# Kernel optimization log

Hardware: AMD Instinct MI355X
Metric: run time of the kernel (lower is better)

The kernel has to match this reference:

```python
import jax, jax.numpy as jnp
import numpy as np

N, E = 50000, 800000
IN_DIM, HID, OUT_DIM = 128, 64, 64
H1, H2 = 4, 2
LRELU_SLOPE = 0.2
LN_EPS = 1e-5


def _glorot(key, shape):
    fan = shape[0] + shape[-1]
    lim = float(np.sqrt(6.0 / fan))
    return jax.random.uniform(key, shape, jnp.float32, -lim, lim)


def setup_inputs() -> dict:
    key = jax.random.key(0)
    ks = jax.random.split(key, 12)
    x = jax.random.normal(ks[0], (N, IN_DIM), jnp.float32)
    edge_index = jax.random.randint(ks[1], (2, E), 0, N, jnp.int64)
    return {
        "x": x,
        "edge_index": edge_index,
        # layer 1: GATConv(128 -> 64, heads=4, concat=True)
        "W1": _glorot(ks[2], (IN_DIM, H1 * HID)),
        "att_src1": _glorot(ks[3], (H1, HID)),
        "att_dst1": _glorot(ks[4], (H1, HID)),
        "b1": jnp.zeros((H1 * HID,), jnp.float32),
        # LayerNorm(256)
        "ln_w": jnp.ones((H1 * HID,), jnp.float32),
        "ln_b": jnp.zeros((H1 * HID,), jnp.float32),
        # layer 2: GATConv(256 -> 64, heads=2, concat=False)
        "W2": _glorot(ks[5], (H1 * HID, H2 * OUT_DIM)),
        "att_src2": _glorot(ks[6], (H2, OUT_DIM)),
        "att_dst2": _glorot(ks[7], (H2, OUT_DIM)),
        "b2": jnp.zeros((OUT_DIM,), jnp.float32),
    }


def gat_layer(x, src, dst, W, a_src, a_dst, bias, heads, out_ch, concat):
    n = x.shape[0]
    h = (x @ W).reshape(n, heads, out_ch)                 # [N,H,C]
    al_s = jnp.einsum("nhc,hc->nh", h, a_src)             # [N,H]
    al_d = jnp.einsum("nhc,hc->nh", h, a_dst)
    e = jax.nn.leaky_relu(al_s[src] + al_d[dst], LRELU_SLOPE)  # [E,H]
    # segment softmax over incoming edges of each dst node
    m = jax.ops.segment_max(e, dst, num_segments=n)
    e = jnp.exp(e - m[dst])
    denom = jax.ops.segment_sum(e, dst, num_segments=n)
    alpha = e / denom[dst]                                # [E,H]
    msg = h[src] * alpha[:, :, None]                      # [E,H,C]
    out = jax.ops.segment_sum(msg, dst, num_segments=n)   # [N,H,C]
    out = out.reshape(n, heads * out_ch) if concat else out.mean(axis=1)
    return out + bias


def layer_norm(x, w, b):
    mu = x.mean(axis=-1, keepdims=True)
    var = ((x - mu) ** 2).mean(axis=-1, keepdims=True)
    return (x - mu) * jax.lax.rsqrt(var + LN_EPS) * w + b


def reference(x, edge_index, W1, att_src1, att_dst1, b1, ln_w, ln_b,
              W2, att_src2, att_dst2, b2):
    # PyG GATConv adds self-loops by default
    loops = jnp.arange(N, dtype=edge_index.dtype)
    src = jnp.concatenate([edge_index[0], loops])
    dst = jnp.concatenate([edge_index[1], loops])
    h = gat_layer(x, src, dst, W1, att_src1, att_dst1, b1, H1, HID, True)
    h = layer_norm(h, ln_w, ln_b)
    h = jax.nn.elu(h)
    # dropout is identity in eval mode
    h = gat_layer(h, src, dst, W2, att_src2, att_dst2, b2, H2, OUT_DIM, False)
    return h
```

## Files before the change

### kernel.cpp

```cpp
#include <hip/hip_runtime.h>
#include <hip/hip_bf16.h>
#include <math.h>

#define IN_DIM  128
#define HID     64
#define H1      4
#define H2      2
#define OUT_DIM 64
#define D1      256
#define D2      128
#define LRELU   0.2f
#define LN_EPS  1e-5f

using short8 = __attribute__((ext_vector_type(8))) short;
using f32x4  = __attribute__((ext_vector_type(4))) float;

static __device__ __forceinline__ unsigned short f2bf_bits(float f)
{
    __hip_bfloat16 b = __float2bfloat16(f);
    return *reinterpret_cast<unsigned short*>(&b);
}
static __device__ __forceinline__ float2 unpack_bf2(unsigned int p)
{
    float2 r;
    r.x = __uint_as_float(p << 16);
    r.y = __uint_as_float(p & 0xffff0000u);
    return r;
}
static __device__ __forceinline__ unsigned int pack_bf2(float x, float y)
{
    return (unsigned int)f2bf_bits(x) | ((unsigned int)f2bf_bits(y) << 16);
}

static __device__ __forceinline__ float lrelu_exp(float v)
{
    v = v > 0.f ? v : LRELU * v;
    return __expf(v);
}

static __device__ __forceinline__ int detect_i64(const int* __restrict__ ei)
{
    int any_odd_nonzero = 0;
    #pragma unroll
    for (int k = 1; k < 16; k += 2) any_odd_nonzero |= (ei[k] != 0);
    return any_odd_nonzero ? 0 : 1;
}

__global__ __launch_bounds__(256) void conv_hist_kernel(
    const float* __restrict__ W1, const float* __restrict__ W2,
    unsigned short* __restrict__ Wp1, unsigned short* __restrict__ Wp2,
    const int* __restrict__ ei, int E, int* __restrict__ deg)
{
    const int bid = blockIdx.x;
    if (bid < 256) {
        int tid = bid * 256 + threadIdx.x;
        if (tid < 32768) {
            int j = tid & 7, l = (tid >> 3) & 63, rest = tid >> 9;
            int s = rest & 15, t = rest >> 4;
            int k = t * 32 + (l >> 4) * 8 + j, col = s * 16 + (l & 15);
            Wp1[tid] = f2bf_bits(W1[k * D1 + col]);
        } else {
            int id = tid - 32768;
            int j = id & 7, l = (id >> 3) & 63, rest = id >> 9;
            int s = rest & 7, t = rest >> 3;
            int k = t * 32 + (l >> 4) * 8 + j, col = s * 16 + (l & 15);
            Wp2[id] = f2bf_bits(W2[k * D2 + col]);
        }
    } else {
        const int i64f = detect_i64(ei);
        int e = (bid - 256) * 256 + threadIdx.x;
        if (e >= E) return;
        int dst = i64f ? ei[2 * ((size_t)E + e)] : ei[E + e];
        atomicAdd(&deg[dst], 1);
    }
}

__global__ __launch_bounds__(256) void scan_gemm1_kernel(
    const int* __restrict__ deg, int N, int* __restrict__ bsum, int scanB,
    const float* __restrict__ x, const unsigned short* __restrict__ Wp,
    const float* __restrict__ att_s, const float* __restrict__ att_d,
    unsigned short* __restrict__ h1b,
    float* __restrict__ al_s, float* __restrict__ al_d)
{
    __shared__ __align__(16) unsigned short As[16 * 136];
    const int tid = threadIdx.x;

    if ((int)blockIdx.x < scanB) {
        int* s = (int*)As;
        int i = blockIdx.x * 256 + tid;
        s[tid] = (i < N) ? deg[i] : 0;
        __syncthreads();
        for (int st = 128; st > 0; st >>= 1) {
            if (tid < st) s[tid] += s[tid + st];
            __syncthreads();
        }
        if (tid == 0) bsum[blockIdx.x] = s[0];
        return;
    }

    const int n0 = ((int)blockIdx.x - scanB) * 16;
    const int l = tid & 63, w = tid >> 6;

    #pragma unroll
    for (int it = 0; it < 2; ++it) {
        int ch = tid + it * 256;
        int r = ch >> 5, c4 = (ch & 31) * 4;
        int row = n0 + r;
        float4 v = (row < N) ? ((const float4*)x)[(size_t)row * 32 + (c4 >> 2)]
                             : make_float4(0.f, 0.f, 0.f, 0.f);
        ushort4 pk = make_ushort4(f2bf_bits(v.x), f2bf_bits(v.y),
                                  f2bf_bits(v.z), f2bf_bits(v.w));
        *(ushort4*)&As[r * 136 + c4] = pk;
    }

    short8 bfr[4][4];
    #pragma unroll
    for (int t = 0; t < 4; ++t)
        #pragma unroll
        for (int p = 0; p < 4; ++p)
            bfr[t][p] = ((const short8*)Wp)[(t * 16 + (w * 4 + p)) * 64 + l];

    __syncthreads();

    f32x4 acc[4] = {{0.f,0.f,0.f,0.f},{0.f,0.f,0.f,0.f},
                    {0.f,0.f,0.f,0.f},{0.f,0.f,0.f,0.f}};
    #pragma unroll
    for (int t = 0; t < 4; ++t) {
        short8 a = *(const short8*)&As[(l & 15) * 136 + t * 32 + (l >> 4) * 8];
        #pragma unroll
        for (int p = 0; p < 4; ++p)
            acc[p] = __builtin_amdgcn_mfma_f32_16x16x32_bf16(a, bfr[t][p], acc[p], 0, 0, 0);
    }

    const int colbase = w * 64 + (l & 15);
    const int rowbase = n0 + (l >> 4) * 4;
    #pragma unroll
    for (int p = 0; p < 4; ++p) {
        int col = colbase + p * 16;
        #pragma unroll
        for (int r = 0; r < 4; ++r) {
            int row = rowbase + r;
            if (row < N) h1b[(size_t)row * D1 + col] = f2bf_bits(acc[p][r]);
        }
    }

    float as_p[4], ad_p[4];
    #pragma unroll
    for (int p = 0; p < 4; ++p) {
        as_p[p] = att_s[colbase + p * 16];
        ad_p[p] = att_d[colbase + p * 16];
    }
    #pragma unroll
    for (int r = 0; r < 4; ++r) {
        float ps = acc[0][r] * as_p[0] + acc[1][r] * as_p[1]
                 + acc[2][r] * as_p[2] + acc[3][r] * as_p[3];
        float pd = acc[0][r] * ad_p[0] + acc[1][r] * ad_p[1]
                 + acc[2][r] * ad_p[2] + acc[3][r] * ad_p[3];
        #pragma unroll
        for (int off = 8; off > 0; off >>= 1) {
            ps += __shfl_down(ps, off);
            pd += __shfl_down(pd, off);
        }
        int row = rowbase + r;
        if ((l & 15) == 0 && row < N) {
            al_s[(size_t)row * H1 + w] = ps;
            al_d[(size_t)row * H1 + w] = pd;
        }
    }
}

__global__ __launch_bounds__(256) void scan_final(
    const int* __restrict__ deg, const int* __restrict__ bsum, int B, int N, int E,
    int* __restrict__ rowptr, int* __restrict__ cursor)
{
    __shared__ int sb[256];
    __shared__ int s[256];
    sb[threadIdx.x] = (threadIdx.x < B) ? bsum[threadIdx.x] : 0;
    __syncthreads();
    for (int st = 1; st < 256; st <<= 1) {
        int t = (threadIdx.x >= st) ? sb[threadIdx.x - st] : 0;
        __syncthreads();
        sb[threadIdx.x] += t;
        __syncthreads();
    }
    const int blockOff = (blockIdx.x == 0) ? 0 : sb[blockIdx.x - 1];

    int i = blockIdx.x * 256 + threadIdx.x;
    int v = (i < N) ? deg[i] : 0;
    s[threadIdx.x] = v;
    __syncthreads();
    for (int st = 1; st < 256; st <<= 1) {
        int t = (threadIdx.x >= st) ? s[threadIdx.x - st] : 0;
        __syncthreads();
        s[threadIdx.x] += t;
        __syncthreads();
    }
    int excl = s[threadIdx.x] - v + blockOff;
    if (i < N) { rowptr[i] = excl; cursor[i] = excl; }
    if (blockIdx.x == 0 && threadIdx.x == 0) rowptr[N] = E;
}

__global__ __launch_bounds__(256) void fill_kernel(
    const int* __restrict__ ei, int E,
    int* __restrict__ cursor, int* __restrict__ csr_src)
{
    const int i64f = detect_i64(ei);
    int e = blockIdx.x * 256 + threadIdx.x;
    if (e >= E) return;
    int src, dst;
    if (i64f) { src = ei[2 * (size_t)e]; dst = ei[2 * ((size_t)E + e)]; }
    else      { src = ei[e];             dst = ei[E + e]; }
    int pos = atomicAdd(&cursor[dst], 1);
    csr_src[pos] = src;
}

__global__ __launch_bounds__(256) void gemm2_mfma(
    const unsigned short* __restrict__ hmidb, const unsigned short* __restrict__ Wp,
    const float* __restrict__ att_s, const float* __restrict__ att_d,
    unsigned short* __restrict__ h2b,
    float* __restrict__ al_s, float* __restrict__ al_d, int N)
{
    __shared__ __align__(16) unsigned short As[16 * 264];
    __shared__ float psL[4][16], pdL[4][16];
    const int tid = threadIdx.x;
    const int n0 = blockIdx.x * 16;
    const int l = tid & 63, w = tid >> 6;

    const short8 zero8 = {0,0,0,0,0,0,0,0};
    #pragma unroll
    for (int it = 0; it < 2; ++it) {
        int ch = tid + it * 256;
        int r = ch >> 5, c8 = (ch & 31) * 8;
        int row = n0 + r;
        short8 v = (row < N) ? ((const short8*)hmidb)[(size_t)row * 32 + (ch & 31)] : zero8;
        *(short8*)&As[r * 264 + c8] = v;
    }

    short8 bfr[8][2];
    #pragma unroll
    for (int t = 0; t < 8; ++t)
        #pragma unroll
        for (int q = 0; q < 2; ++q)
            bfr[t][q] = ((const short8*)Wp)[(t * 8 + (w * 2 + q)) * 64 + l];

    __syncthreads();

    f32x4 acc[2] = {{0.f,0.f,0.f,0.f},{0.f,0.f,0.f,0.f}};
    #pragma unroll
    for (int t = 0; t < 8; ++t) {
        short8 a = *(const short8*)&As[(l & 15) * 264 + t * 32 + (l >> 4) * 8];
        #pragma unroll
        for (int q = 0; q < 2; ++q)
            acc[q] = __builtin_amdgcn_mfma_f32_16x16x32_bf16(a, bfr[t][q], acc[q], 0, 0, 0);
    }

    const int colbase = w * 32 + (l & 15);
    const int rowbase = n0 + (l >> 4) * 4;
    #pragma unroll
    for (int q = 0; q < 2; ++q) {
        int col = colbase + q * 16;
        #pragma unroll
        for (int r = 0; r < 4; ++r) {
            int row = rowbase + r;
            if (row < N) h2b[(size_t)row * D2 + col] = f2bf_bits(acc[q][r]);
        }
    }

    float as_q[2], ad_q[2];
    #pragma unroll
    for (int q = 0; q < 2; ++q) {
        as_q[q] = att_s[colbase + q * 16];
        ad_q[q] = att_d[colbase + q * 16];
    }
    #pragma unroll
    for (int r = 0; r < 4; ++r) {
        float ps = acc[0][r] * as_q[0] + acc[1][r] * as_q[1];
        float pd = acc[0][r] * ad_q[0] + acc[1][r] * ad_q[1];
        #pragma unroll
        for (int off = 8; off > 0; off >>= 1) {
            ps += __shfl_down(ps, off);
            pd += __shfl_down(pd, off);
        }
        if ((l & 15) == 0) {
            psL[w][(l >> 4) * 4 + r] = ps;
            pdL[w][(l >> 4) * 4 + r] = pd;
        }
    }
    __syncthreads();
    if (tid < 32) {
        int rl = tid & 15, hh = tid >> 4;
        int row = n0 + rl;
        if (row < N) {
            al_s[(size_t)row * H2 + hh] = psL[2*hh][rl] + psL[2*hh+1][rl];
            al_d[(size_t)row * H2 + hh] = pdL[2*hh][rl] + pdL[2*hh+1][rl];
        }
    }
}

__global__ __launch_bounds__(64) void agg1_kernel(
    const int* __restrict__ rowptr, const int* __restrict__ csr_src,
    const uint2* __restrict__ h1p,
    const float* __restrict__ al_s, const float* __restrict__ al_d,
    const float* __restrict__ b1,
    const float* __restrict__ ln_w, const float* __restrict__ ln_b,
    uint2* __restrict__ hmidp, int N)
{
    const int n = blockIdx.x;
    const int l = threadIdx.x;
    const int h = l >> 4;
    const float ad = al_d[(size_t)n * H1 + h];

    float a0[4] = {0.f,0.f,0.f,0.f}, a1[4] = {0.f,0.f,0.f,0.f};
    float a2[4] = {0.f,0.f,0.f,0.f}, a3[4] = {0.f,0.f,0.f,0.f};
    float dn0, dn1 = 0.f, dn2 = 0.f, dn3 = 0.f;

    {
        float w = lrelu_exp(al_s[(size_t)n * H1 + h] + ad);
        uint2 p = h1p[(size_t)n * 64 + l];
        float2 va = unpack_bf2(p.x), vb = unpack_bf2(p.y);
        a0[0] = w * va.x; a0[1] = w * va.y; a0[2] = w * vb.x; a0[3] = w * vb.y;
        dn0 = w;
    }

    const int beg = rowptr[n], end = rowptr[n + 1];
    int i = beg;

#define LOADI(k)  int s##k = csr_src[i + k];
#define LOADR(k)  uint2 p##k = h1p[(size_t)s##k * 64 + l]; \
                  float g##k = al_s[(size_t)s##k * H1 + h];
#define WACC(A, D, k) { float w = lrelu_exp(g##k + ad); \
                        float2 va = unpack_bf2(p##k.x), vb = unpack_bf2(p##k.y); \
                        A[0] += w * va.x; A[1] += w * va.y; \
                        A[2] += w * vb.x; A[3] += w * vb.y; D += w; }

    for (; i + 4 <= end; i += 4) {
        LOADI(0) LOADI(1) LOADI(2) LOADI(3)
        LOADR(0) LOADR(1) LOADR(2) LOADR(3)
        WACC(a0, dn0, 0) WACC(a1, dn1, 1) WACC(a2, dn2, 2) WACC(a3, dn3, 3)
    }
    for (; i < end; ++i) {
        LOADI(0) LOADR(0) WACC(a0, dn0, 0)
    }
#undef LOADI
#undef LOADR
#undef WACC

    const float inv = 1.f / ((dn0 + dn1) + (dn2 + dn3));
    float4 bb = ((const float4*)b1)[l];
    float v[4];
    v[0] = ((a0[0]+a1[0]) + (a2[0]+a3[0])) * inv + bb.x;
    v[1] = ((a0[1]+a1[1]) + (a2[1]+a3[1])) * inv + bb.y;
    v[2] = ((a0[2]+a1[2]) + (a2[2]+a3[2])) * inv + bb.z;
    v[3] = ((a0[3]+a1[3]) + (a2[3]+a3[3])) * inv + bb.w;

    float s  = (v[0]+v[1]) + (v[2]+v[3]);
    float s2 = (v[0]*v[0]+v[1]*v[1]) + (v[2]*v[2]+v[3]*v[3]);
    #pragma unroll
    for (int off = 32; off > 0; off >>= 1) {
        s  += __shfl_down(s,  off);
        s2 += __shfl_down(s2, off);
    }
    const float mu   = __shfl(s,  0) * (1.f / 256.f);
    const float ex2  = __shfl(s2, 0) * (1.f / 256.f);
    const float rstd = rsqrtf(ex2 - mu * mu + LN_EPS);
    float4 lw = ((const float4*)ln_w)[l];
    float4 lb = ((const float4*)ln_b)[l];
    float y0 = (v[0] - mu) * rstd * lw.x + lb.x;
    float y1 = (v[1] - mu) * rstd * lw.y + lb.y;
    float y2 = (v[2] - mu) * rstd * lw.z + lb.z;
    float y3 = (v[3] - mu) * rstd * lw.w + lb.w;
    y0 = y0 > 0.f ? y0 : (__expf(y0) - 1.f);
    y1 = y1 > 0.f ? y1 : (__expf(y1) - 1.f);
    y2 = y2 > 0.f ? y2 : (__expf(y2) - 1.f);
    y3 = y3 > 0.f ? y3 : (__expf(y3) - 1.f);
    uint2 outp;
    outp.x = pack_bf2(y0, y1);
    outp.y = pack_bf2(y2, y3);
    hmidp[(size_t)n * 64 + l] = outp;
}

__global__ __launch_bounds__(64) void agg2_kernel(
    const int* __restrict__ rowptr, const int* __restrict__ csr_src,
    const unsigned int* __restrict__ h2p,
    const float* __restrict__ al_s, const float* __restrict__ al_d,
    const float* __restrict__ b2,
    float* __restrict__ out, int N)
{
    const int n = blockIdx.x;
    const int l = threadIdx.x;
    const int h = l >> 5;
    const float ad = al_d[(size_t)n * H2 + h];

    float ax0, ay0, dn0;
    float ax1 = 0.f, ay1 = 0.f, dn1 = 0.f;
    float ax2 = 0.f, ay2 = 0.f, dn2 = 0.f;
    float ax3 = 0.f, ay3 = 0.f, dn3 = 0.f;
    {
        float w = lrelu_exp(al_s[(size_t)n * H2 + h] + ad);
        float2 hv = unpack_bf2(h2p[(size_t)n * 64 + l]);
        ax0 = w * hv.x; ay0 = w * hv.y; dn0 = w;
    }

    const int beg = rowptr[n], end = rowptr[n + 1];
    int i = beg;

#define LOADI(k)  int s##k = csr_src[i + k];
#define LOADR(k)  unsigned int p##k = h2p[(size_t)s##k * 64 + l]; \
                  float g##k = al_s[(size_t)s##k * H2 + h];
#define WACC(AX, AY, D, k) { float w = lrelu_exp(g##k + ad); \
                             float2 vv = unpack_bf2(p##k); \
                             AX += w * vv.x; AY += w * vv.y; D += w; }

    for (; i + 4 <= end; i += 4) {
        LOADI(0) LOADI(1) LOADI(2) LOADI(3)
        LOADR(0) LOADR(1) LOADR(2) LOADR(3)
        WACC(ax0, ay0, dn0, 0) WACC(ax1, ay1, dn1, 1)
        WACC(ax2, ay2, dn2, 2) WACC(ax3, ay3, dn3, 3)
    }
    for (; i < end; ++i) {
        LOADI(0) LOADR(0) WACC(ax0, ay0, dn0, 0)
    }
#undef LOADI
#undef LOADR
#undef WACC

    const float inv = 1.f / ((dn0 + dn1) + (dn2 + dn3));
    const float vx = ((ax0 + ax1) + (ax2 + ax3)) * inv;
    const float vy = ((ay0 + ay1) + (ay2 + ay3)) * inv;

    const float vx1 = __shfl(vx, l + 32);
    const float vy1 = __shfl(vy, l + 32);
    if (l < 32) {
        float2 bb = ((const float2*)b2)[l];
        float2 o;
        o.x = 0.5f * (vx + vx1) + bb.x;
        o.y = 0.5f * (vy + vy1) + bb.y;
        ((float2*)out)[(size_t)n * 32 + l] = o;
    }
}

extern "C" void kernel_launch(void* const* d_in, const int* in_sizes, int n_in,
                              void* d_out, int out_size, void* d_ws, size_t ws_size,
                              hipStream_t stream)
{
    const float* x   = (const float*)d_in[0];
    const int*   ei  = (const int*)d_in[1];
    const float* W1  = (const float*)d_in[2];
    const float* as1 = (const float*)d_in[3];
    const float* ad1 = (const float*)d_in[4];
    const float* b1  = (const float*)d_in[5];
    const float* lnw = (const float*)d_in[6];
    const float* lnb = (const float*)d_in[7];
    const float* W2  = (const float*)d_in[8];
    const float* as2 = (const float*)d_in[9];
    const float* ad2 = (const float*)d_in[10];
    const float* b2  = (const float*)d_in[11];

    const int N = in_sizes[0] / IN_DIM;
    const int E = in_sizes[1] / 2;

    char* ws = (char*)d_ws;
    const size_t szH1b = (size_t)N * D1 * sizeof(unsigned short);
    unsigned short* h1b   = (unsigned short*)(ws);
    unsigned short* hmidb = (unsigned short*)(ws + szH1b);
    unsigned short* Wp1   = (unsigned short*)(ws + 2 * szH1b);
    unsigned short* Wp2   = Wp1 + 32768;
    float* al_s1 = (float*)(Wp2 + 32768);
    float* al_d1 = al_s1 + (size_t)N * H1;
    float* al_s2 = al_d1 + (size_t)N * H1;
    float* al_d2 = al_s2 + (size_t)N * H2;
    int* deg     = (int*)(al_d2 + (size_t)N * H2);
    int* rowptr  = deg + (N + 1);
    int* cursor  = rowptr + (N + 1);
    int* csr_src = cursor + (N + 1);
    int* bsum    = csr_src + E;
    unsigned short* h2b = h1b;

    hipMemsetAsync(deg, 0, (size_t)(N + 1) * sizeof(int), stream);

    const int edgeBlocks = (E + 255) / 256;
    const int scanBlocks = (N + 255) / 256;
    const int tileBlocks = (N + 15) / 16;

    conv_hist_kernel<<<256 + edgeBlocks, 256, 0, stream>>>(W1, W2, Wp1, Wp2, ei, E, deg);
    scan_gemm1_kernel<<<scanBlocks + tileBlocks, 256, 0, stream>>>(
        deg, N, bsum, scanBlocks, x, Wp1, as1, ad1, h1b, al_s1, al_d1);
    scan_final<<<scanBlocks, 256, 0, stream>>>(deg, bsum, scanBlocks, N, E, rowptr, cursor);
    fill_kernel<<<edgeBlocks, 256, 0, stream>>>(ei, E, cursor, csr_src);

    agg1_kernel<<<N, 64, 0, stream>>>(rowptr, csr_src, (const uint2*)h1b,
                                      al_s1, al_d1, b1, lnw, lnb,
                                      (uint2*)hmidb, N);
    gemm2_mfma<<<tileBlocks, 256, 0, stream>>>(hmidb, Wp2, as2, ad2, h2b, al_s2, al_d2, N);
    agg2_kernel<<<N, 64, 0, stream>>>(rowptr, csr_src, (const unsigned int*)h2b,
                                      al_s2, al_d2, b2, (float*)d_out, N);
}
```

Before: 311.7 us.

## Build CSR via two-level bucket scatter with shared-memory atomics

Replaces the single-pass CSR fill, which did one global atomic per edge on a per-node cursor and a random write, with two passes. First, edges are packed as (src<<16|dst) and scattered into 64-node buckets using per-bucket global atomics. Then one block per bucket places sources into final CSR positions using LDS atomics, so the writes stay local. This aims to improve locality of the scatter writes, but adds a kernel launch, an extra pass over the edges, and heavier contention on the much smaller set of bucket counters. The packing also assumes node ids below 65536.

```diff
diff --git a/kernel.cpp b/kernel.cpp
--- a/kernel.cpp
+++ b/kernel.cpp
@@ -171,7 +171,7 @@
 
 __global__ __launch_bounds__(256) void scan_final(
     const int* __restrict__ deg, const int* __restrict__ bsum, int B, int N, int E,
-    int* __restrict__ rowptr, int* __restrict__ cursor)
+    int* __restrict__ rowptr, int* __restrict__ boff, int* __restrict__ bcur)
 {
     __shared__ int sb[256];
     __shared__ int s[256];
@@ -196,13 +196,19 @@
         __syncthreads();
     }
     int excl = s[threadIdx.x] - v + blockOff;
-    if (i < N) { rowptr[i] = excl; cursor[i] = excl; }
-    if (blockIdx.x == 0 && threadIdx.x == 0) rowptr[N] = E;
-}
-
-__global__ __launch_bounds__(256) void fill_kernel(
+    if (i < N) {
+        rowptr[i] = excl;
+        if ((i & 63) == 0) { boff[i >> 6] = excl; bcur[i >> 6] = excl; }
+    }
+    if (blockIdx.x == 0 && threadIdx.x == 0) {
+        rowptr[N] = E;
+        boff[(N + 63) >> 6] = E;
+    }
+}
+
+__global__ __launch_bounds__(256) void bucket_scatter(
     const int* __restrict__ ei, int E,
-    int* __restrict__ cursor, int* __restrict__ csr_src)
+    int* __restrict__ bcur, unsigned int* __restrict__ pairs)
 {
     const int i64f = detect_i64(ei);
     int e = blockIdx.x * 256 + threadIdx.x;
@@ -210,8 +216,29 @@
     int src, dst;
     if (i64f) { src = ei[2 * (size_t)e]; dst = ei[2 * ((size_t)E + e)]; }
     else      { src = ei[e];             dst = ei[E + e]; }
-    int pos = atomicAdd(&cursor[dst], 1);
-    csr_src[pos] = src;
+    int pos = atomicAdd(&bcur[dst >> 6], 1);
+    pairs[pos] = ((unsigned int)src << 16) | (unsigned int)dst;
+}
+
+__global__ __launch_bounds__(256) void fill2_kernel(
+    const unsigned int* __restrict__ pairs, const int* __restrict__ boff,
+    const int* __restrict__ rowptr, int N,
+    int* __restrict__ csr_src)
+{
+    __shared__ int cur[64];
+    const int b = blockIdx.x;
+    const int t = threadIdx.x;
+    if (t < 64) {
+        int node = b * 64 + t;
+        cur[t] = (node < N) ? rowptr[node] : 0;
+    }
+    __syncthreads();
+    const int beg = boff[b], end = boff[b + 1];
+    for (int i = beg + t; i < end; i += 256) {
+        unsigned int p = pairs[i];
+        int pos = atomicAdd(&cur[p & 63], 1);
+        csr_src[pos] = (int)(p >> 16);
+    }
 }
 
 __global__ __launch_bounds__(256) void gemm2_mfma(
@@ -471,9 +498,12 @@
     float* al_d2 = al_s2 + (size_t)N * H2;
     int* deg     = (int*)(al_d2 + (size_t)N * H2);
     int* rowptr  = deg + (N + 1);
-    int* cursor  = rowptr + (N + 1);
-    int* csr_src = cursor + (N + 1);
+    int* csr_src = rowptr + (N + 1);
     int* bsum    = csr_src + E;
+    const int nb = (N + 63) >> 6;
+    int* boff    = bsum + 256;
+    int* bcur    = boff + (nb + 1);
+    unsigned int* pairs = (unsigned int*)(bcur + nb);
     unsigned short* h2b = h1b;
 
     hipMemsetAsync(deg, 0, (size_t)(N + 1) * sizeof(int), stream);
@@ -485,8 +515,10 @@
     conv_hist_kernel<<<256 + edgeBlocks, 256, 0, stream>>>(W1, W2, Wp1, Wp2, ei, E, deg);
     scan_gemm1_kernel<<<scanBlocks + tileBlocks, 256, 0, stream>>>(
         deg, N, bsum, scanBlocks, x, Wp1, as1, ad1, h1b, al_s1, al_d1);
-    scan_final<<<scanBlocks, 256, 0, stream>>>(deg, bsum, scanBlocks, N, E, rowptr, cursor);
-    fill_kernel<<<edgeBlocks, 256, 0, stream>>>(ei, E, cursor, csr_src);
+    scan_final<<<scanBlocks, 256, 0, stream>>>(deg, bsum, scanBlocks, N, E,
+                                               rowptr, boff, bcur);
+    bucket_scatter<<<edgeBlocks, 256, 0, stream>>>(ei, E, bcur, pairs);
+    fill2_kernel<<<nb, 256, 0, stream>>>(pairs, boff, rowptr, N, csr_src);
 
     agg1_kernel<<<N, 64, 0, stream>>>(rowptr, csr_src, (const uint2*)h1b,
                                       al_s1, al_d1, b1, lnw, lnb,
```

Result: slower. 455.9 us (+46.3%).

## Build CSR via two-level bucketed scatter with shared-memory local sort

Applied to the files above, without the earlier changes.

Replaces the single-pass per-edge atomic CSR fill with a two-level scheme. Edges are first scattered into 16-node buckets, split into 8 sub-streams by edge block, as packed (src,dst) pairs. A per-bucket kernel then places them into final positions using shared-memory atomics and staging. This aims to cut global atomic contention and scattered writes, at the cost of an extra pass over the edges, an extra kernel launch and a second histogram. Packing src into 16 bits assumes N < 65536, and the dst & 15 bucket index relies on buckets being 16-aligned.

```diff
diff --git a/kernel.cpp b/kernel.cpp
--- a/kernel.cpp
+++ b/kernel.cpp
@@ -11,6 +11,7 @@
 #define D2      128
 #define LRELU   0.2f
 #define LN_EPS  1e-5f
+#define BK      16
 
 using short8 = __attribute__((ext_vector_type(8))) short;
 using f32x4  = __attribute__((ext_vector_type(4))) float;
@@ -49,7 +50,7 @@
 __global__ __launch_bounds__(256) void conv_hist_kernel(
     const float* __restrict__ W1, const float* __restrict__ W2,
     unsigned short* __restrict__ Wp1, unsigned short* __restrict__ Wp2,
-    const int* __restrict__ ei, int E, int* __restrict__ deg)
+    const int* __restrict__ ei, int E, int* __restrict__ deg, int* __restrict__ sdeg)
 {
     const int bid = blockIdx.x;
     if (bid < 256) {
@@ -72,6 +73,7 @@
         if (e >= E) return;
         int dst = i64f ? ei[2 * ((size_t)E + e)] : ei[E + e];
         atomicAdd(&deg[dst], 1);
+        atomicAdd(&sdeg[(dst / BK) * 8 + ((e >> 8) & 7)], 1);
     }
 }
 
@@ -171,10 +173,12 @@
 
 __global__ __launch_bounds__(256) void scan_final(
     const int* __restrict__ deg, const int* __restrict__ bsum, int B, int N, int E,
-    int* __restrict__ rowptr, int* __restrict__ cursor)
+    const int* __restrict__ sdeg, int NB,
+    int* __restrict__ rowptr, int* __restrict__ bcur)
 {
     __shared__ int sb[256];
     __shared__ int s[256];
+    __shared__ int exc[256];
     sb[threadIdx.x] = (threadIdx.x < B) ? bsum[threadIdx.x] : 0;
     __syncthreads();
     for (int st = 1; st < 256; st <<= 1) {
@@ -196,13 +200,26 @@
         __syncthreads();
     }
     int excl = s[threadIdx.x] - v + blockOff;
-    if (i < N) { rowptr[i] = excl; cursor[i] = excl; }
+    exc[threadIdx.x] = excl;
+    if (i < N) rowptr[i] = excl;
     if (blockIdx.x == 0 && threadIdx.x == 0) rowptr[N] = E;
-}
-
-__global__ __launch_bounds__(256) void fill_kernel(
+    __syncthreads();
+
+    if (threadIdx.x < 128) {
+        int bl = threadIdx.x >> 3, st = threadIdx.x & 7;
+        int b = blockIdx.x * 16 + bl;
+        if (b < NB) {
+            int base = exc[bl * BK];
+            int pre = 0;
+            for (int s2 = 0; s2 < st; ++s2) pre += sdeg[b * 8 + s2];
+            bcur[b * 8 + st] = base + pre;
+        }
+    }
+}
+
+__global__ __launch_bounds__(256) void bucket_scatter(
     const int* __restrict__ ei, int E,
-    int* __restrict__ cursor, int* __restrict__ csr_src)
+    int* __restrict__ bcur, unsigned int* __restrict__ pairs)
 {
     const int i64f = detect_i64(ei);
     int e = blockIdx.x * 256 + threadIdx.x;
@@ -210,8 +227,45 @@
     int src, dst;
     if (i64f) { src = ei[2 * (size_t)e]; dst = ei[2 * ((size_t)E + e)]; }
     else      { src = ei[e];             dst = ei[E + e]; }
-    int pos = atomicAdd(&cursor[dst], 1);
-    csr_src[pos] = src;
+    int pos = atomicAdd(&bcur[(dst / BK) * 8 + ((e >> 8) & 7)], 1);
+    pairs[pos] = ((unsigned int)src << 16) | (unsigned int)dst;
+}
+
+__global__ __launch_bounds__(256) void fill2_kernel(
+    const unsigned int* __restrict__ pairs, const int* __restrict__ rowptr,
+    int N, int NB, int* __restrict__ csr_src)
+{
+    __shared__ int cur[BK];
+    __shared__ int stage[2048];
+    const int b = blockIdx.x;
+    const int t = threadIdx.x;
+    const int base = rowptr[b * BK];
+    const int endn = (b * BK + BK < N) ? (b * BK + BK) : N;
+    const int segend = rowptr[endn];
+    const int seglen = segend - base;
+
+    if (t < BK) {
+        int node = b * BK + t;
+        cur[t] = ((node < N) ? rowptr[node] : segend) - base;
+    }
+    __syncthreads();
+
+    if (seglen <= 2048) {
+        for (int i = t; i < seglen; i += 256) {
+            unsigned int p = pairs[base + i];
+            int pos = atomicAdd(&cur[p & (BK - 1)], 1);
+            stage[pos] = (int)(p >> 16);
+        }
+        __syncthreads();
+        for (int i = t; i < seglen; i += 256)
+            csr_src[base + i] = stage[i];
+    } else {
+        for (int i = t; i < seglen; i += 256) {
+            unsigned int p = pairs[base + i];
+            int pos = atomicAdd(&cur[p & (BK - 1)], 1);
+            csr_src[base + pos] = (int)(p >> 16);
+        }
+    }
 }
 
 __global__ __launch_bounds__(256) void gemm2_mfma(
@@ -458,6 +512,7 @@
 
     const int N = in_sizes[0] / IN_DIM;
     const int E = in_sizes[1] / 2;
+    const int NB = (N + BK - 1) / BK;
 
     char* ws = (char*)d_ws;
     const size_t szH1b = (size_t)N * D1 * sizeof(unsigned short);
@@ -470,23 +525,27 @@
     float* al_s2 = al_d1 + (size_t)N * H1;
     float* al_d2 = al_s2 + (size_t)N * H2;
     int* deg     = (int*)(al_d2 + (size_t)N * H2);
-    int* rowptr  = deg + (N + 1);
-    int* cursor  = rowptr + (N + 1);
-    int* csr_src = cursor + (N + 1);
+    int* sdeg    = deg + (N + 1);
+    int* rowptr  = sdeg + NB * 8;
+    int* bcur    = rowptr + (N + 1);
+    int* csr_src = bcur + NB * 8;
     int* bsum    = csr_src + E;
+    unsigned int* pairs = (unsigned int*)(bsum + 256);
     unsigned short* h2b = h1b;
 
-    hipMemsetAsync(deg, 0, (size_t)(N + 1) * sizeof(int), stream);
+    hipMemsetAsync(deg, 0, (size_t)(N + 1 + NB * 8) * sizeof(int), stream);
 
     const int edgeBlocks = (E + 255) / 256;
     const int scanBlocks = (N + 255) / 256;
     const int tileBlocks = (N + 15) / 16;
 
-    conv_hist_kernel<<<256 + edgeBlocks, 256, 0, stream>>>(W1, W2, Wp1, Wp2, ei, E, deg);
+    conv_hist_kernel<<<256 + edgeBlocks, 256, 0, stream>>>(W1, W2, Wp1, Wp2, ei, E, deg, sdeg);
     scan_gemm1_kernel<<<scanBlocks + tileBlocks, 256, 0, stream>>>(
         deg, N, bsum, scanBlocks, x, Wp1, as1, ad1, h1b, al_s1, al_d1);
-    scan_final<<<scanBlocks, 256, 0, stream>>>(deg, bsum, scanBlocks, N, E, rowptr, cursor);
-    fill_kernel<<<edgeBlocks, 256, 0, stream>>>(ei, E, cursor, csr_src);
+    scan_final<<<scanBlocks, 256, 0, stream>>>(deg, bsum, scanBlocks, N, E,
+                                               sdeg, NB, rowptr, bcur);
+    bucket_scatter<<<edgeBlocks, 256, 0, stream>>>(ei, E, bcur, pairs);
+    fill2_kernel<<<NB, 256, 0, stream>>>(pairs, rowptr, N, NB, csr_src);
 
     agg1_kernel<<<N, 64, 0, stream>>>(rowptr, csr_src, (const uint2*)h1b,
                                       al_s1, al_d1, b1, lnw, lnb,
```

Result: slower. 343.4 us (+10.2%).
